# Kernel optimization log

Measured on AMD Instinct MI355X. Metric: run time of the kernel, lower is better.

## Reference

```python
import jax, jax.numpy as jnp
import numpy as np

N = 50000      # nodes
D = 3          # relations (len(edges_set))
E = 800000     # edges per relation
IN, HID, OUT = 300, 256, 256
NEG_SLOPE = 0.2


def _xavier(key, shape):
    fan_in, fan_out = shape
    lim = float(np.sqrt(6.0 / (fan_in + fan_out)))
    return jax.random.uniform(key, shape, jnp.float32, -lim, lim)


def _spmm(rows, cols, vals, x):
    # y[rows] += vals * x[cols] ; sparse (COO) @ dense
    return jax.ops.segment_sum(x[cols] * vals[:, None], rows, num_segments=N)


def setup_inputs() -> dict:
    key = jax.random.key(0)
    ks = jax.random.split(key, 8)
    src = jax.random.randint(ks[0], (D, E), 0, N, dtype=jnp.int32)
    dst = jax.random.randint(ks[1], (D, E), 0, N, dtype=jnp.int32)
    ones = jnp.ones((E,), jnp.float32)
    # normt_spm(adj, 'in')  == rownorm(A^T): edge val 1/indeg(dst), row index = dst
    # normt_spm(adj.T, 'in')== rownorm(A):   edge val 1/outdeg(src), row index = src
    indeg = jax.vmap(lambda d: jax.ops.segment_sum(ones, d, num_segments=N))(dst)
    outdeg = jax.vmap(lambda s: jax.ops.segment_sum(ones, s, num_segments=N))(src)
    vals_a = 1.0 / jnp.take_along_axis(indeg, dst, axis=1)   # [D, E]
    vals_r = 1.0 / jnp.take_along_axis(outdeg, src, axis=1)  # [D, E]
    x = jax.random.normal(ks[2], (N, IN), jnp.float32)
    w1 = _xavier(ks[3], (IN, HID))
    b1 = jnp.zeros((HID,), jnp.float32)
    w2 = _xavier(ks[4], (HID, OUT))
    b2 = jnp.zeros((OUT,), jnp.float32)
    a_att = jnp.ones((D,), jnp.float32)
    r_att = jnp.ones((D,), jnp.float32)
    return dict(x=x, w1=w1, b1=b1, w2=w2, b2=b2, a_att=a_att, r_att=r_att,
                src=src, dst=dst, vals_a=vals_a, vals_r=vals_r)


def reference(x, w1, b1, w2, b2, a_att, r_att, src, dst, vals_a, vals_r):
    # layer 1 (graph side: a_adj set, a_att)
    att = jax.nn.softmax(a_att)
    s = x @ w1 + b1
    h = att[0] * _spmm(dst[0], src[0], vals_a[0], s)
    for i in range(1, D):
        h = h + att[i] * _spmm(dst[i], src[i], vals_a[i], s)
    h = jnp.where(h > 0, h, NEG_SLOPE * h)  # LeakyReLU(0.2)
    # layer 2 (reverse side: r_adj set, r_att; no relu)
    att2 = jax.nn.softmax(r_att)
    s2 = h @ w2 + b2
    out = att2[0] * _spmm(src[0], dst[0], vals_r[0], s2)
    for i in range(1, D):
        out = out + att2[i] * _spmm(src[i], dst[i], vals_r[i], s2)
    # F.normalize: row-wise L2, eps=1e-12
    norm = jnp.linalg.norm(out, axis=1, keepdims=True)
    return out / jnp.maximum(norm, 1e-12)
```

## Files before the change

### kernel.cpp

```cpp
#include <hip/hip_runtime.h>
#include <stdint.h>

#define NN 50000
#define NRELS 3
#define NE 800000
#define DIN 300
#define KP 320
#define DH 256
#define NBUK 196
#define NBT (6*NBUK)
#define PAD 16
#define CAP 5120
#define CHUNK 4096
#define NLB 392

typedef __attribute__((ext_vector_type(8))) short bf16x8;
typedef __attribute__((ext_vector_type(4))) float f32x4;

__device__ __forceinline__ float bf2f(unsigned short u){
    union { unsigned int i; float f; } v; v.i = ((unsigned int)u) << 16; return v.f;
}
__device__ __forceinline__ unsigned short f2bf(float f){
    union { float f; unsigned int i; } v; v.f = f;
    return (unsigned short)((v.i + 0x7FFFu + ((v.i >> 16) & 1u)) >> 16);
}

__global__ void k_att(const float* __restrict__ a_att, const float* __restrict__ r_att,
                      float* __restrict__ att){
    if (threadIdx.x == 0){
        float m = fmaxf(a_att[0], fmaxf(a_att[1], a_att[2]));
        float e0 = expf(a_att[0]-m), e1 = expf(a_att[1]-m), e2 = expf(a_att[2]-m);
        float s = e0+e1+e2;
        att[0]=e0/s; att[1]=e1/s; att[2]=e2/s;
        m = fmaxf(r_att[0], fmaxf(r_att[1], r_att[2]));
        e0 = expf(r_att[0]-m); e1 = expf(r_att[1]-m); e2 = expf(r_att[2]-m);
        s = e0+e1+e2;
        att[3]=e0/s; att[4]=e1/s; att[5]=e2/s;
    }
}

__global__ void k_binit(int* __restrict__ bcur){
    int b = blockIdx.x*256 + threadIdx.x;
    if (b < NBT) bcur[b*PAD] = b*CAP;
}

__global__ __launch_bounds__(256) void k_bscatter_agg(const int* __restrict__ src,
                                                      const int* __restrict__ dst,
                                                      int* __restrict__ bcur,
                                                      unsigned int* __restrict__ bucketbuf){
    __shared__ unsigned int ledge[2*CHUNK];
    __shared__ unsigned short lbid[2*CHUNK];
    __shared__ int lhist[448];
    __shared__ int lstart[NLB];
    __shared__ int gbase[NLB];
    __shared__ int glim[NLB];
    const int rel = blockIdx.y;
    const int e0 = blockIdx.x*CHUNK;
    const int tid = threadIdx.x;
    for (int i = tid; i < 448; i += 256) lhist[i] = 0;
    __syncthreads();
    int sv[16], dv[16];
    #pragma unroll
    for (int j = 0; j < 16; ++j){
        int e = e0 + j*256 + tid;
        if (e < NE){
            sv[j] = src[(size_t)rel*NE + e];
            dv[j] = dst[(size_t)rel*NE + e];
            atomicAdd(&lhist[dv[j] >> 8], 1);
            atomicAdd(&lhist[196 + (sv[j] >> 8)], 1);
        } else sv[j] = -1;
    }
    __syncthreads();
    if (tid < 64){
        int base = tid*7, s = 0, tmp[7];
        #pragma unroll
        for (int j = 0; j < 7; ++j){ tmp[j] = s; s += lhist[base+j]; }
        int run = s;
        #pragma unroll
        for (int off_ = 1; off_ < 64; off_ <<= 1){
            int t = __shfl_up(run, off_);
            if (tid >= off_) run += t;
        }
        int excl = run - s;
        #pragma unroll
        for (int j = 0; j < 7; ++j) lhist[base+j] = tmp[j] + excl;
    }
    __syncthreads();
    for (int i = tid; i < NLB; i += 256) lstart[i] = lhist[i];
    __syncthreads();
    #pragma unroll
    for (int j = 0; j < 16; ++j){
        if (sv[j] >= 0){
            int lb = dv[j] >> 8;
            int pos = atomicAdd(&lhist[lb], 1);
            ledge[pos] = ((unsigned)(dv[j] & 255) << 16) | (unsigned)sv[j];
            lbid[pos] = (unsigned short)lb;
            lb = 196 + (sv[j] >> 8);
            pos = atomicAdd(&lhist[lb], 1);
            ledge[pos] = ((unsigned)(sv[j] & 255) << 16) | (unsigned)dv[j];
            lbid[pos] = (unsigned short)lb;
        }
    }
    __syncthreads();
    for (int lb = tid; lb < NLB; lb += 256){
        int cnt = lhist[lb] - lstart[lb];
        if (cnt > 0){
            int gb = (lb < 196) ? (rel*NBUK + lb) : ((NRELS+rel)*NBUK + lb - 196);
            int base = atomicAdd(&bcur[gb*PAD], cnt);
            gbase[lb] = base;
            glim[lb]  = min(base + cnt, gb*CAP + CAP);
        }
    }
    __syncthreads();
    const int total = min(NE - e0, CHUNK)*2;
    for (int i = tid; i < total; i += 256){
        int lb = lbid[i];
        int dest = gbase[lb] + (i - lstart[lb]);
        if (dest < glim[lb]) bucketbuf[dest] = ledge[i];
    }
}

__global__ __launch_bounds__(256) void k_bfinal(const unsigned int* __restrict__ bucketbuf,
                                                const int* __restrict__ bcur,
                                                int* __restrict__ row_start,
                                                int* __restrict__ row_end,
                                                unsigned short* __restrict__ colS){
    __shared__ int lhist[256];
    __shared__ int lcur[256];
    __shared__ unsigned int ledge[CAP];
    int b = blockIdx.x;
    int a = b / NBUK, bu = b % NBUK;
    int row0 = bu << 8;
    int base = b*CAP;
    int cnt = min(bcur[b*PAD] - base, CAP);
    int tid = threadIdx.x;
    lhist[tid] = 0;
    __syncthreads();
    for (int i = tid; i < cnt; i += 256){
        unsigned int p = bucketbuf[base + i];
        ledge[i] = p;
        atomicAdd(&lhist[p >> 16], 1);
    }
    __syncthreads();
    int v = lhist[tid];
    for (int off_ = 1; off_ < 256; off_ <<= 1){
        int t = (tid >= off_) ? lhist[tid - off_] : 0;
        __syncthreads();
        lhist[tid] += t;
        __syncthreads();
    }
    int excl = lhist[tid] - v;
    lcur[tid] = excl;
    int rows = NN - row0; if (rows > 256) rows = 256;
    if (tid < rows){
        row_start[a*NN + row0 + tid] = base + excl;
        row_end[a*NN + row0 + tid]   = base + excl + v;
    }
    __syncthreads();
    for (int i = tid; i < cnt; i += 256){
        unsigned int p = ledge[i];
        int pos = atomicAdd(&lcur[p >> 16], 1);
        colS[base + pos] = (unsigned short)(p & 0xFFFFu);
    }
}

__global__ void k_w1t(const float* __restrict__ w1, unsigned short* __restrict__ w1t){
    int idx = blockIdx.x*256 + threadIdx.x;
    int n = idx / KP, k = idx % KP;
    w1t[idx] = (k < DIN) ? f2bf(w1[(size_t)k*DH + n]) : 0;
}

__global__ void k_w2t(const float* __restrict__ w2, unsigned short* __restrict__ w2t){
    int idx = blockIdx.x*256 + threadIdx.x;
    int n = idx >> 8, k = idx & 255;
    w2t[idx] = f2bf(w2[k*DH + n]);
}

__global__ __launch_bounds__(256) void k_gemm1(const float* __restrict__ x,
                                               const unsigned short* __restrict__ w1t,
                                               const float* __restrict__ bias,
                                               unsigned short* __restrict__ out, int M){
    const int wave = threadIdx.x >> 6;
    const int lane = threadIdx.x & 63;
    const int row0 = (blockIdx.x*4 + wave) * 16;
    if (row0 >= M) return;
    const int r = lane & 15;
    const int g = lane >> 4;
    const float* xrow = x + (size_t)(row0 + r)*DIN;
    f32x4 acc[16];
    #pragma unroll
    for (int n = 0; n < 16; ++n) acc[n] = (f32x4){0.f,0.f,0.f,0.f};
    #pragma unroll
    for (int kk = 0; kk < KP/32; ++kk){
        const int k0 = kk*32 + g*8;
        bf16x8 a;
        if (kk < 9){
            float4 xa = *(const float4*)(xrow + k0);
            float4 xb = *(const float4*)(xrow + k0 + 4);
            a[0]=(short)f2bf(xa.x); a[1]=(short)f2bf(xa.y);
            a[2]=(short)f2bf(xa.z); a[3]=(short)f2bf(xa.w);
            a[4]=(short)f2bf(xb.x); a[5]=(short)f2bf(xb.y);
            a[6]=(short)f2bf(xb.z); a[7]=(short)f2bf(xb.w);
        } else {
            #pragma unroll
            for (int j = 0; j < 8; ++j){
                int k = k0 + j;
                a[j] = (short)((k < DIN) ? f2bf(xrow[k]) : 0);
            }
        }
        #pragma unroll
        for (int n = 0; n < 16; ++n){
            bf16x8 bfr = *(const bf16x8*)(w1t + (size_t)(n*16 + r)*KP + kk*32 + g*8);
            acc[n] = __builtin_amdgcn_mfma_f32_16x16x32_bf16(a, bfr, acc[n], 0, 0, 0);
        }
    }
    #pragma unroll
    for (int n = 0; n < 16; ++n){
        float bv = bias[n*16 + r];
        #pragma unroll
        for (int j = 0; j < 4; ++j){
            int row = row0 + g*4 + j;
            out[(size_t)row*DH + n*16 + r] = f2bf(acc[n][j] + bv);
        }
    }
}

__global__ __launch_bounds__(256) void k_gemm2(const unsigned short* __restrict__ h,
                                               const unsigned short* __restrict__ w2t,
                                               const float* __restrict__ bias,
                                               unsigned short* __restrict__ out, int M){
    const int wave = threadIdx.x >> 6;
    const int lane = threadIdx.x & 63;
    const int row0 = (blockIdx.x*4 + wave) * 16;
    if (row0 >= M) return;
    const int r = lane & 15;
    const int g = lane >> 4;
    f32x4 acc[16];
    #pragma unroll
    for (int n = 0; n < 16; ++n) acc[n] = (f32x4){0.f,0.f,0.f,0.f};
    #pragma unroll
    for (int kk = 0; kk < DH/32; ++kk){
        const int k0 = kk*32;
        bf16x8 a = *(const bf16x8*)(h + (size_t)(row0 + r)*DH + k0 + g*8);
        #pragma unroll
        for (int n = 0; n < 16; ++n){
            bf16x8 bfr = *(const bf16x8*)(w2t + (size_t)(n*16 + r)*DH + k0 + g*8);
            acc[n] = __builtin_amdgcn_mfma_f32_16x16x32_bf16(a, bfr, acc[n], 0, 0, 0);
        }
    }
    #pragma unroll
    for (int n = 0; n < 16; ++n){
        float bv = bias[n*16 + r];
        #pragma unroll
        for (int j = 0; j < 4; ++j){
            int row = row0 + g*4 + j;
            out[(size_t)row*DH + n*16 + r] = f2bf(acc[n][j] + bv);
        }
    }
}

#define GATHER_ACC(U) \
    t0 += bf2f((U).x); t1 += bf2f((U).y); t2 += bf2f((U).z); t3 += bf2f((U).w);

__global__ __launch_bounds__(256) void k_spmm1(const unsigned short* __restrict__ feat,
                                               const int* __restrict__ row_start,
                                               const int* __restrict__ row_end,
                                               const unsigned short* __restrict__ colS,
                                               const float* __restrict__ att,
                                               unsigned short* __restrict__ out){
    int row = __builtin_amdgcn_readfirstlane(blockIdx.x*4 + (threadIdx.x >> 6));
    int lane = threadIdx.x & 63;
    if (row >= NN) return;
    const size_t loff = (size_t)lane*4;
    float a0=0.f, a1=0.f, a2=0.f, a3=0.f;
    #pragma unroll
    for (int i = 0; i < NRELS; ++i){
        const int s0 = row_start[i*NN + row];
        const int s1 = row_end[i*NN + row];
        const int n = s1 - s0;
        if (n <= 0) continue;
        float t0=0.f, t1=0.f, t2=0.f, t3=0.f;
        int slot = s0;
        for (; slot + 8 <= s1; slot += 8){
            int c0 = colS[slot+0], c1 = colS[slot+1], c2 = colS[slot+2], c3 = colS[slot+3];
            int c4 = colS[slot+4], c5 = colS[slot+5], c6 = colS[slot+6], c7 = colS[slot+7];
            ushort4 u0 = *(const ushort4*)(feat + (size_t)c0*DH + loff);
            ushort4 u1 = *(const ushort4*)(feat + (size_t)c1*DH + loff);
            ushort4 u2 = *(const ushort4*)(feat + (size_t)c2*DH + loff);
            ushort4 u3 = *(const ushort4*)(feat + (size_t)c3*DH + loff);
            ushort4 u4 = *(const ushort4*)(feat + (size_t)c4*DH + loff);
            ushort4 u5 = *(const ushort4*)(feat + (size_t)c5*DH + loff);
            ushort4 u6 = *(const ushort4*)(feat + (size_t)c6*DH + loff);
            ushort4 u7 = *(const ushort4*)(feat + (size_t)c7*DH + loff);
            GATHER_ACC(u0) GATHER_ACC(u1) GATHER_ACC(u2) GATHER_ACC(u3)
            GATHER_ACC(u4) GATHER_ACC(u5) GATHER_ACC(u6) GATHER_ACC(u7)
        }
        for (; slot < s1; ++slot){
            int c = colS[slot];
            ushort4 u = *(const ushort4*)(feat + (size_t)c*DH + loff);
            GATHER_ACC(u)
        }
        float v = att[i] / (float)n;
        a0 += v*t0; a1 += v*t1; a2 += v*t2; a3 += v*t3;
    }
    a0 = a0 > 0.f ? a0 : 0.2f*a0;
    a1 = a1 > 0.f ? a1 : 0.2f*a1;
    a2 = a2 > 0.f ? a2 : 0.2f*a2;
    a3 = a3 > 0.f ? a3 : 0.2f*a3;
    ushort4 o; o.x = f2bf(a0); o.y = f2bf(a1); o.z = f2bf(a2); o.w = f2bf(a3);
    *(ushort4*)(&out[(size_t)row*DH + loff]) = o;
}

__global__ __launch_bounds__(256) void k_spmm2(const unsigned short* __restrict__ feat,
                                               const int* __restrict__ row_start,
                                               const int* __restrict__ row_end,
                                               const unsigned short* __restrict__ colS,
                                               const float* __restrict__ att,
                                               float* __restrict__ out){
    int row = __builtin_amdgcn_readfirstlane(blockIdx.x*4 + (threadIdx.x >> 6));
    int lane = threadIdx.x & 63;
    if (row >= NN) return;
    const size_t loff = (size_t)lane*4;
    float a0=0.f, a1=0.f, a2=0.f, a3=0.f;
    #pragma unroll
    for (int i = 0; i < NRELS; ++i){
        const int a = NRELS + i;
        const int s0 = row_start[a*NN + row];
        const int s1 = row_end[a*NN + row];
        const int n = s1 - s0;
        if (n <= 0) continue;
        float t0=0.f, t1=0.f, t2=0.f, t3=0.f;
        int slot = s0;
        for (; slot + 8 <= s1; slot += 8){
            int c0 = colS[slot+0], c1 = colS[slot+1], c2 = colS[slot+2], c3 = colS[slot+3];
            int c4 = colS[slot+4], c5 = colS[slot+5], c6 = colS[slot+6], c7 = colS[slot+7];
            ushort4 u0 = *(const ushort4*)(feat + (size_t)c0*DH + loff);
            ushort4 u1 = *(const ushort4*)(feat + (size_t)c1*DH + loff);
            ushort4 u2 = *(const ushort4*)(feat + (size_t)c2*DH + loff);
            ushort4 u3 = *(const ushort4*)(feat + (size_t)c3*DH + loff);
            ushort4 u4 = *(const ushort4*)(feat + (size_t)c4*DH + loff);
            ushort4 u5 = *(const ushort4*)(feat + (size_t)c5*DH + loff);
            ushort4 u6 = *(const ushort4*)(feat + (size_t)c6*DH + loff);
            ushort4 u7 = *(const ushort4*)(feat + (size_t)c7*DH + loff);
            GATHER_ACC(u0) GATHER_ACC(u1) GATHER_ACC(u2) GATHER_ACC(u3)
            GATHER_ACC(u4) GATHER_ACC(u5) GATHER_ACC(u6) GATHER_ACC(u7)
        }
        for (; slot < s1; ++slot){
            int c = colS[slot];
            ushort4 u = *(const ushort4*)(feat + (size_t)c*DH + loff);
            GATHER_ACC(u)
        }
        float v = att[a] / (float)n;
        a0 += v*t0; a1 += v*t1; a2 += v*t2; a3 += v*t3;
    }
    float ss = a0*a0 + a1*a1 + a2*a2 + a3*a3;
    #pragma unroll
    for (int off = 32; off > 0; off >>= 1) ss += __shfl_xor(ss, off);
    float scale = 1.0f / fmaxf(sqrtf(ss), 1e-12f);
    float4 o; o.x = a0*scale; o.y = a1*scale; o.z = a2*scale; o.w = a3*scale;
    *(float4*)(&out[(size_t)row*DH + loff]) = o;
}

extern "C" void kernel_launch(void* const* d_in, const int* in_sizes, int n_in,
                              void* d_out, int out_size, void* d_ws, size_t ws_size,
                              hipStream_t stream){
    const float* x      = (const float*)d_in[0];
    const float* w1     = (const float*)d_in[1];
    const float* b1     = (const float*)d_in[2];
    const float* w2     = (const float*)d_in[3];
    const float* b2     = (const float*)d_in[4];
    const float* a_att  = (const float*)d_in[5];
    const float* r_att  = (const float*)d_in[6];
    const int*   src    = (const int*)d_in[7];
    const int*   dst    = (const int*)d_in[8];
    float* out = (float*)d_out;

    char* ws = (char*)d_ws;
    size_t off = 0;
    auto take = [&](size_t bytes)->char*{
        char* p = ws + off;
        off = (off + bytes + 255) & ~(size_t)255;
        return p;
    };
    float*          att         = (float*)take(6*sizeof(float));
    unsigned short* sbuf        = (unsigned short*)take((size_t)NN*DH*2);
    unsigned short* hbuf        = (unsigned short*)take((size_t)NN*DH*2);
    unsigned short* w1t         = (unsigned short*)take((size_t)DH*KP*2);
    unsigned short* w2t         = (unsigned short*)take((size_t)DH*DH*2);
    int*            bcur        = (int*)take((size_t)NBT*PAD*4);
    int*            row_start   = (int*)take((size_t)6*NN*4);
    int*            row_end     = (int*)take((size_t)6*NN*4);
    unsigned int*   bucketbuf   = (unsigned int*)take((size_t)NBT*CAP*4);
    unsigned short* colS        = (unsigned short*)take((size_t)NBT*CAP*2);
    (void)ws_size; (void)in_sizes; (void)n_in; (void)out_size;

    k_att<<<1, 64, 0, stream>>>(a_att, r_att, att);
    k_w1t<<<(DH*KP + 255)/256, 256, 0, stream>>>(w1, w1t);
    k_w2t<<<(DH*DH + 255)/256, 256, 0, stream>>>(w2, w2t);
    k_binit<<<(NBT + 255)/256, 256, 0, stream>>>(bcur);

    dim3 sgrid((NE + CHUNK - 1)/CHUNK, NRELS);
    k_bscatter_agg<<<sgrid, 256, 0, stream>>>(src, dst, bcur, bucketbuf);
    k_bfinal<<<NBT, 256, 0, stream>>>(bucketbuf, bcur, row_start, row_end, colS);

    k_gemm1<<<(NN/16 + 3)/4, 256, 0, stream>>>(x, w1t, b1, sbuf, NN);
    k_spmm1<<<(NN + 3)/4, 256, 0, stream>>>(sbuf, row_start, row_end, colS, att, hbuf);

    k_gemm2<<<(NN/16 + 3)/4, 256, 0, stream>>>(hbuf, w2t, b2, sbuf, NN);
    k_spmm2<<<(NN + 3)/4, 256, 0, stream>>>(sbuf, row_start, row_end, colS, att, out);
}
```

Baseline: 695.4 us.

## Merge relation buckets into per-row CSR with int4 metadata and fused prep

Reorganizes the CSR build so that all three relations for a given 256-row bucket are sorted together into one contiguous segment. Each row now gets an int4 giving the start offsets of its three relation sub-ranges. The SpMM kernels then walk a single merged edge range per row, selecting a per-edge weight and using fmaf, instead of three separate short loops with tail handling. This is meant to cut loop overhead and tail inefficiency and to keep more gathers in flight. The four small prep kernels are also fused into one launch to remove launch overhead; the cost is extra per-edge weight-select arithmetic and a larger shared histogram in the finalize kernel.

```diff
diff --git a/kernel.cpp b/kernel.cpp
--- a/kernel.cpp
+++ b/kernel.cpp
@@ -11,6 +11,7 @@
 #define NBT (6*NBUK)
 #define PAD 16
 #define CAP 5120
+#define MCAP (3*CAP)
 #define CHUNK 4096
 #define NLB 392
 
@@ -25,9 +26,23 @@
     return (unsigned short)((v.i + 0x7FFFu + ((v.i >> 16) & 1u)) >> 16);
 }
 
-__global__ void k_att(const float* __restrict__ a_att, const float* __restrict__ r_att,
-                      float* __restrict__ att){
-    if (threadIdx.x == 0){
+__global__ void k_prep(const float* __restrict__ w1, const float* __restrict__ w2,
+                       const float* __restrict__ a_att, const float* __restrict__ r_att,
+                       unsigned short* __restrict__ w1t, unsigned short* __restrict__ w2t,
+                       int* __restrict__ bcur, float* __restrict__ att){
+    int b = blockIdx.x, tid = threadIdx.x;
+    if (b < 320){
+        int idx = b*256 + tid;
+        int n = idx / KP, k = idx % KP;
+        w1t[idx] = (k < DIN) ? f2bf(w1[(size_t)k*DH + n]) : 0;
+    } else if (b < 576){
+        int idx = (b-320)*256 + tid;
+        int n = idx >> 8, k = idx & 255;
+        w2t[idx] = f2bf(w2[k*DH + n]);
+    } else if (b < 581){
+        int i = (b-576)*256 + tid;
+        if (i < NBT) bcur[i*PAD] = i*CAP;
+    } else if (tid == 0){
         float m = fmaxf(a_att[0], fmaxf(a_att[1], a_att[2]));
         float e0 = expf(a_att[0]-m), e1 = expf(a_att[1]-m), e2 = expf(a_att[2]-m);
         float s = e0+e1+e2;
@@ -37,11 +52,6 @@
         s = e0+e1+e2;
         att[3]=e0/s; att[4]=e1/s; att[5]=e2/s;
     }
-}
-
-__global__ void k_binit(int* __restrict__ bcur){
-    int b = blockIdx.x*256 + threadIdx.x;
-    if (b < NBT) bcur[b*PAD] = b*CAP;
 }
 
 __global__ __launch_bounds__(256) void k_bscatter_agg(const int* __restrict__ src,
@@ -93,11 +103,11 @@
         if (sv[j] >= 0){
             int lb = dv[j] >> 8;
             int pos = atomicAdd(&lhist[lb], 1);
-            ledge[pos] = ((unsigned)(dv[j] & 255) << 16) | (unsigned)sv[j];
+            ledge[pos] = ((unsigned)dv[j] << 16) | (unsigned)sv[j];
             lbid[pos] = (unsigned short)lb;
             lb = 196 + (sv[j] >> 8);
             pos = atomicAdd(&lhist[lb], 1);
-            ledge[pos] = ((unsigned)(sv[j] & 255) << 16) | (unsigned)dv[j];
+            ledge[pos] = ((unsigned)sv[j] << 16) | (unsigned)dv[j];
             lbid[pos] = (unsigned short)lb;
         }
     }
@@ -122,58 +132,72 @@
 
 __global__ __launch_bounds__(256) void k_bfinal(const unsigned int* __restrict__ bucketbuf,
                                                 const int* __restrict__ bcur,
-                                                int* __restrict__ row_start,
-                                                int* __restrict__ row_end,
+                                                int4* __restrict__ rowmeta,
                                                 unsigned short* __restrict__ colS){
-    __shared__ int lhist[256];
-    __shared__ int lcur[256];
-    __shared__ unsigned int ledge[CAP];
-    int b = blockIdx.x;
-    int a = b / NBUK, bu = b % NBUK;
-    int row0 = bu << 8;
-    int base = b*CAP;
-    int cnt = min(bcur[b*PAD] - base, CAP);
-    int tid = threadIdx.x;
-    lhist[tid] = 0;
-    __syncthreads();
-    for (int i = tid; i < cnt; i += 256){
-        unsigned int p = bucketbuf[base + i];
-        ledge[i] = p;
-        atomicAdd(&lhist[p >> 16], 1);
-    }
-    __syncthreads();
-    int v = lhist[tid];
-    for (int off_ = 1; off_ < 256; off_ <<= 1){
-        int t = (tid >= off_) ? lhist[tid - off_] : 0;
-        __syncthreads();
-        lhist[tid] += t;
-        __syncthreads();
-    }
-    int excl = lhist[tid] - v;
-    lcur[tid] = excl;
+    __shared__ int lhist[1024];
+    __shared__ int lcur[1024];
+    __shared__ int wtot[4];
+    const int b = blockIdx.x;
+    const int a2 = b / NBUK, bu = b % NBUK;
+    const int row0 = bu << 8;
+    const int obase = b * MCAP;
+    const int tid = threadIdx.x;
+    for (int i = tid; i < 1024; i += 256) lhist[i] = 0;
+    __syncthreads();
+    int srcb[3], scnt[3];
+    #pragma unroll
+    for (int i = 0; i < 3; ++i){
+        int gb = (a2*NRELS + i)*NBUK + bu;
+        srcb[i] = gb*CAP;
+        scnt[i] = min(bcur[gb*PAD] - srcb[i], CAP);
+    }
+    #pragma unroll
+    for (int i = 0; i < 3; ++i){
+        for (int j = tid; j < scnt[i]; j += 256){
+            unsigned p = bucketbuf[srcb[i] + j];
+            atomicAdd(&lhist[(((p >> 16) & 255) << 2) | i], 1);
+        }
+    }
+    __syncthreads();
+    int c0 = lhist[4*tid], c1 = lhist[4*tid+1], c2 = lhist[4*tid+2];
+    int tsum = c0 + c1 + c2;
+    int lane = tid & 63, wv = tid >> 6;
+    int incl = tsum;
+    #pragma unroll
+    for (int off_ = 1; off_ < 64; off_ <<= 1){
+        int t = __shfl_up(incl, off_);
+        if (lane >= off_) incl += t;
+    }
+    if (lane == 63) wtot[wv] = incl;
+    __syncthreads();
+    int woff = 0;
+    #pragma unroll
+    for (int w = 0; w < 4; ++w) woff += (w < wv) ? wtot[w] : 0;
+    int toff = woff + incl - tsum;
+    lhist[4*tid]   = toff;
+    lhist[4*tid+1] = toff + c0;
+    lhist[4*tid+2] = toff + c0 + c1;
+    lcur[4*tid]    = toff;
+    lcur[4*tid+1]  = toff + c0;
+    lcur[4*tid+2]  = toff + c0 + c1;
     int rows = NN - row0; if (rows > 256) rows = 256;
     if (tid < rows){
-        row_start[a*NN + row0 + tid] = base + excl;
-        row_end[a*NN + row0 + tid]   = base + excl + v;
-    }
-    __syncthreads();
-    for (int i = tid; i < cnt; i += 256){
-        unsigned int p = ledge[i];
-        int pos = atomicAdd(&lcur[p >> 16], 1);
-        colS[base + pos] = (unsigned short)(p & 0xFFFFu);
-    }
-}
-
-__global__ void k_w1t(const float* __restrict__ w1, unsigned short* __restrict__ w1t){
-    int idx = blockIdx.x*256 + threadIdx.x;
-    int n = idx / KP, k = idx % KP;
-    w1t[idx] = (k < DIN) ? f2bf(w1[(size_t)k*DH + n]) : 0;
-}
-
-__global__ void k_w2t(const float* __restrict__ w2, unsigned short* __restrict__ w2t){
-    int idx = blockIdx.x*256 + threadIdx.x;
-    int n = idx >> 8, k = idx & 255;
-    w2t[idx] = f2bf(w2[k*DH + n]);
+        int4 m;
+        m.x = obase + toff;
+        m.y = obase + toff + c0;
+        m.z = obase + toff + c0 + c1;
+        m.w = obase + toff + c0 + c1 + c2;
+        rowmeta[a2*NN + row0 + tid] = m;
+    }
+    __syncthreads();
+    #pragma unroll
+    for (int i = 0; i < 3; ++i){
+        for (int j = tid; j < scnt[i]; j += 256){
+            unsigned p = bucketbuf[srcb[i] + j];
+            int pos = atomicAdd(&lcur[(((p >> 16) & 255) << 2) | i], 1);
+            colS[obase + pos] = (unsigned short)(p & 0xFFFFu);
+        }
+    }
 }
 
 __global__ __launch_bounds__(256) void k_gemm1(const float* __restrict__ x,
@@ -259,12 +283,33 @@
     }
 }
 
-#define GATHER_ACC(U) \
-    t0 += bf2f((U).x); t1 += bf2f((U).y); t2 += bf2f((U).z); t3 += bf2f((U).w);
+#define SPMM_BODY(M_, ACCUM)                                                         \
+    const int e = M_.w;                                                              \
+    int slot = M_.x;                                                                 \
+    if (e > slot){                                                                   \
+        const int e1 = e - 1;                                                        \
+        for (; slot < e; slot += 8){                                                 \
+            int cc[8]; float vv[8];                                                  \
+            _Pragma("unroll")                                                        \
+            for (int j = 0; j < 8; ++j){                                             \
+                int sj = slot + j;                                                   \
+                cc[j] = colS[min(sj, e1)];                                           \
+                float v = (sj < M_.y) ? v0 : ((sj < M_.z) ? v1 : v2);                \
+                vv[j] = (sj < e) ? v : 0.f;                                          \
+            }                                                                        \
+            _Pragma("unroll")                                                        \
+            for (int j = 0; j < 8; ++j){                                             \
+                ushort4 u = *(const ushort4*)(feat + (size_t)cc[j]*DH + loff);       \
+                ACCUM(u, vv[j])                                                      \
+            }                                                                        \
+        }                                                                            \
+    }
+#define ACC4(U, V) \
+    a0 = fmaf(V, bf2f((U).x), a0); a1 = fmaf(V, bf2f((U).y), a1); \
+    a2 = fmaf(V, bf2f((U).z), a2); a3 = fmaf(V, bf2f((U).w), a3);
 
 __global__ __launch_bounds__(256) void k_spmm1(const unsigned short* __restrict__ feat,
-                                               const int* __restrict__ row_start,
-                                               const int* __restrict__ row_end,
+                                               const int4* __restrict__ rowmeta,
                                                const unsigned short* __restrict__ colS,
                                                const float* __restrict__ att,
                                                unsigned short* __restrict__ out){
@@ -272,37 +317,12 @@
     int lane = threadIdx.x & 63;
     if (row >= NN) return;
     const size_t loff = (size_t)lane*4;
+    int4 m = rowmeta[row];
+    float v0 = att[0] / (float)max(m.y - m.x, 1);
+    float v1 = att[1] / (float)max(m.z - m.y, 1);
+    float v2 = att[2] / (float)max(m.w - m.z, 1);
     float a0=0.f, a1=0.f, a2=0.f, a3=0.f;
-    #pragma unroll
-    for (int i = 0; i < NRELS; ++i){
-        const int s0 = row_start[i*NN + row];
-        const int s1 = row_end[i*NN + row];
-        const int n = s1 - s0;
-        if (n <= 0) continue;
-        float t0=0.f, t1=0.f, t2=0.f, t3=0.f;
-        int slot = s0;
-        for (; slot + 8 <= s1; slot += 8){
-            int c0 = colS[slot+0], c1 = colS[slot+1], c2 = colS[slot+2], c3 = colS[slot+3];
-            int c4 = colS[slot+4], c5 = colS[slot+5], c6 = colS[slot+6], c7 = colS[slot+7];
-            ushort4 u0 = *(const ushort4*)(feat + (size_t)c0*DH + loff);
-            ushort4 u1 = *(const ushort4*)(feat + (size_t)c1*DH + loff);
-            ushort4 u2 = *(const ushort4*)(feat + (size_t)c2*DH + loff);
-            ushort4 u3 = *(const ushort4*)(feat + (size_t)c3*DH + loff);
-            ushort4 u4 = *(const ushort4*)(feat + (size_t)c4*DH + loff);
-            ushort4 u5 = *(const ushort4*)(feat + (size_t)c5*DH + loff);
-            ushort4 u6 = *(const ushort4*)(feat + (size_t)c6*DH + loff);
-            ushort4 u7 = *(const ushort4*)(feat + (size_t)c7*DH + loff);
-            GATHER_ACC(u0) GATHER_ACC(u1) GATHER_ACC(u2) GATHER_ACC(u3)
-            GATHER_ACC(u4) GATHER_ACC(u5) GATHER_ACC(u6) GATHER_ACC(u7)
-        }
-        for (; slot < s1; ++slot){
-            int c = colS[slot];
-            ushort4 u = *(const ushort4*)(feat + (size_t)c*DH + loff);
-            GATHER_ACC(u)
-        }
-        float v = att[i] / (float)n;
-        a0 += v*t0; a1 += v*t1; a2 += v*t2; a3 += v*t3;
-    }
+    SPMM_BODY(m, ACC4)
     a0 = a0 > 0.f ? a0 : 0.2f*a0;
     a1 = a1 > 0.f ? a1 : 0.2f*a1;
     a2 = a2 > 0.f ? a2 : 0.2f*a2;
@@ -312,8 +332,7 @@
 }
 
 __global__ __launch_bounds__(256) void k_spmm2(const unsigned short* __restrict__ feat,
-                                               const int* __restrict__ row_start,
-                                               const int* __restrict__ row_end,
+                                               const int4* __restrict__ rowmeta,
                                                const unsigned short* __restrict__ colS,
                                                const float* __restrict__ att,
                                                float* __restrict__ out){
@@ -321,38 +340,12 @@
     int lane = threadIdx.x & 63;
     if (row >= NN) return;
     const size_t loff = (size_t)lane*4;
+    int4 m = rowmeta[NN + row];
+    float v0 = att[3] / (float)max(m.y - m.x, 1);
+    float v1 = att[4] / (float)max(m.z - m.y, 1);
+    float v2 = att[5] / (float)max(m.w - m.z, 1);
     float a0=0.f, a1=0.f, a2=0.f, a3=0.f;
-    #pragma unroll
-    for (int i = 0; i < NRELS; ++i){
-        const int a = NRELS + i;
-        const int s0 = row_start[a*NN + row];
-        const int s1 = row_end[a*NN + row];
-        const int n = s1 - s0;
-        if (n <= 0) continue;
-        float t0=0.f, t1=0.f, t2=0.f, t3=0.f;
-        int slot = s0;
-        for (; slot + 8 <= s1; slot += 8){
-            int c0 = colS[slot+0], c1 = colS[slot+1], c2 = colS[slot+2], c3 = colS[slot+3];
-            int c4 = colS[slot+4], c5 = colS[slot+5], c6 = colS[slot+6], c7 = colS[slot+7];
-            ushort4 u0 = *(const ushort4*)(feat + (size_t)c0*DH + loff);
-            ushort4 u1 = *(const ushort4*)(feat + (size_t)c1*DH + loff);
-            ushort4 u2 = *(const ushort4*)(feat + (size_t)c2*DH + loff);
-            ushort4 u3 = *(const ushort4*)(feat + (size_t)c3*DH + loff);
-            ushort4 u4 = *(const ushort4*)(feat + (size_t)c4*DH + loff);
-            ushort4 u5 = *(const ushort4*)(feat + (size_t)c5*DH + loff);
-            ushort4 u6 = *(const ushort4*)(feat + (size_t)c6*DH + loff);
-            ushort4 u7 = *(const ushort4*)(feat + (size_t)c7*DH + loff);
-            GATHER_ACC(u0) GATHER_ACC(u1) GATHER_ACC(u2) GATHER_ACC(u3)
-            GATHER_ACC(u4) GATHER_ACC(u5) GATHER_ACC(u6) GATHER_ACC(u7)
-        }
-        for (; slot < s1; ++slot){
-            int c = colS[slot];
-            ushort4 u = *(const ushort4*)(feat + (size_t)c*DH + loff);
-            GATHER_ACC(u)
-        }
-        float v = att[a] / (float)n;
-        a0 += v*t0; a1 += v*t1; a2 += v*t2; a3 += v*t3;
-    }
+    SPMM_BODY(m, ACC4)
     float ss = a0*a0 + a1*a1 + a2*a2 + a3*a3;
     #pragma unroll
     for (int off = 32; off > 0; off >>= 1) ss += __shfl_xor(ss, off);
@@ -388,24 +381,20 @@
     unsigned short* w1t         = (unsigned short*)take((size_t)DH*KP*2);
     unsigned short* w2t         = (unsigned short*)take((size_t)DH*DH*2);
     int*            bcur        = (int*)take((size_t)NBT*PAD*4);
-    int*            row_start   = (int*)take((size_t)6*NN*4);
-    int*            row_end     = (int*)take((size_t)6*NN*4);
+    int4*           rowmeta     = (int4*)take((size_t)2*NN*16);
     unsigned int*   bucketbuf   = (unsigned int*)take((size_t)NBT*CAP*4);
-    unsigned short* colS        = (unsigned short*)take((size_t)NBT*CAP*2);
+    unsigned short* colS        = (unsigned short*)take((size_t)2*NBUK*MCAP*2);
     (void)ws_size; (void)in_sizes; (void)n_in; (void)out_size;
 
-    k_att<<<1, 64, 0, stream>>>(a_att, r_att, att);
-    k_w1t<<<(DH*KP + 255)/256, 256, 0, stream>>>(w1, w1t);
-    k_w2t<<<(DH*DH + 255)/256, 256, 0, stream>>>(w2, w2t);
-    k_binit<<<(NBT + 255)/256, 256, 0, stream>>>(bcur);
+    k_prep<<<582, 256, 0, stream>>>(w1, w2, a_att, r_att, w1t, w2t, bcur, att);
 
     dim3 sgrid((NE + CHUNK - 1)/CHUNK, NRELS);
     k_bscatter_agg<<<sgrid, 256, 0, stream>>>(src, dst, bcur, bucketbuf);
-    k_bfinal<<<NBT, 256, 0, stream>>>(bucketbuf, bcur, row_start, row_end, colS);
+    k_bfinal<<<2*NBUK, 256, 0, stream>>>(bucketbuf, bcur, rowmeta, colS);
 
     k_gemm1<<<(NN/16 + 3)/4, 256, 0, stream>>>(x, w1t, b1, sbuf, NN);
-    k_spmm1<<<(NN + 3)/4, 256, 0, stream>>>(sbuf, row_start, row_end, colS, att, hbuf);
+    k_spmm1<<<(NN + 3)/4, 256, 0, stream>>>(sbuf, rowmeta, colS, att, hbuf);
 
     k_gemm2<<<(NN/16 + 3)/4, 256, 0, stream>>>(hbuf, w2t, b2, sbuf, NN);
-    k_spmm2<<<(NN + 3)/4, 256, 0, stream>>>(sbuf, row_start, row_end, colS, att, out);
-}
+    k_spmm2<<<(NN + 3)/4, 256, 0, stream>>>(sbuf, rowmeta, colS, att, out);
+}
```

After: 690.6 us. Within noise of the previous version (-0.7%).
